# Kernel tuning notes

Hardware: AMD Instinct MI355X
Metric: run time of the kernel (lower is better)

The kernel has to match this reference:

```python
import jax, jax.numpy as jnp
import numpy as np

TOP_K = 4  # matches init kwarg top_k


def setup_inputs() -> dict:
    key = jax.random.key(0)
    k1, k2 = jax.random.split(key)
    G, S, D, E = 4, 2048, 1024, 32
    x = jax.random.normal(k1, (G, S, D), dtype=jnp.float32)
    W = jax.random.normal(k2, (D, E), dtype=jnp.float32) * (1.0 / np.sqrt(D))
    b = jnp.zeros((E,), dtype=jnp.float32)
    return {"x": x, "W": W, "b": b, "expert_capacity": 256}


def reference(x, W, b, expert_capacity):
    # gating_logits: [G, S, E]
    gating_logits = jnp.einsum('gsd,de->gse', x, W) + b
    gating_probs = jax.nn.softmax(gating_logits, axis=-1)
    # top-k gate values and expert indices: [G, S, K]
    expert_gate, expert_index = jax.lax.top_k(gating_probs, TOP_K)
    E = gating_probs.shape[2]
    # one-hot expert mask: [G, S, K, E]
    expert_mask = jax.nn.one_hot(expert_index, num_classes=E, dtype=gating_probs.dtype)
    # position of each assignment within its expert (1-based where assigned)
    position_in_expert = jnp.cumsum(expert_mask, axis=1) * expert_mask  # [G,S,K,E]
    valid_assignment = position_in_expert < expert_capacity
    expert_gate_valid = expert_gate[..., None] * valid_assignment.astype(expert_gate.dtype)
    # one-hot over capacity slots: [G,S,K,E,C]
    combine_per_assignment = expert_gate_valid[..., None] * jax.nn.one_hot(
        position_in_expert, num_classes=expert_capacity, dtype=expert_gate.dtype)
    combine_tensor = jnp.sum(combine_per_assignment, axis=2)  # [G,S,E,C]
    combine_tensor = combine_tensor[..., 1:]                  # drop slot 0 (unassigned)
    dispatch_mask = combine_tensor.astype(bool)
    loss = 0.0  # training=False
    return combine_tensor, dispatch_mask, loss
```

## Files before the change

kernel.cpp:

```cpp
#include <hip/hip_runtime.h>

#define G 4
#define S 2048
#define D 1024
#define E 32
#define TOPK 4
#define NTOK (G * S)
#define NROW (NTOK * E)
#define ROWLEN 255
#define HALF (NROW * ROWLEN)


__global__ __launch_bounds__(256) void gemm_topk_kernel(
    const float* __restrict__ x, const float* __restrict__ W,
    const float* __restrict__ b,
    float* __restrict__ gate_ws, int* __restrict__ idx_ws,
    int2* __restrict__ tab)
{
    const int tid   = threadIdx.x;
    const int token = blockIdx.x * 8 + (tid >> 5);
    const int e     = tid & 31;

    tab[token * E + e] = make_int2(0, 0);

    const float4* x4 = (const float4*)x;
    const long xb = (long)token * (D / 4);

    float acc = 0.f;
#pragma unroll 4
    for (int d4 = 0; d4 < D / 4; ++d4) {
        float4 xv = x4[xb + d4];
        const float* wp = W + d4 * 4 * E + e;
        acc = fmaf(xv.x, wp[0],     acc);
        acc = fmaf(xv.y, wp[E],     acc);
        acc = fmaf(xv.z, wp[2 * E], acc);
        acc = fmaf(xv.w, wp[3 * E], acc);
    }
    acc += b[e];

    float m = acc;
#pragma unroll
    for (int off = 16; off >= 1; off >>= 1)
        m = fmaxf(m, __shfl_xor(m, off, 32));
    float ex = __expf(acc - m);
    float sum = ex;
#pragma unroll
    for (int off = 16; off >= 1; off >>= 1)
        sum += __shfl_xor(sum, off, 32);
    float prob = ex / sum;

    const int g = token >> 11;
    const int s = token & (S - 1);

    float p = prob;
#pragma unroll
    for (int kk = 0; kk < TOPK; ++kk) {
        float v = p;
        int   vi = e;
#pragma unroll
        for (int off = 16; off >= 1; off >>= 1) {
            float ov = __shfl_xor(v, off, 32);
            int   oi = __shfl_xor(vi, off, 32);
            if (ov > v || (ov == v && oi < vi)) { v = ov; vi = oi; }
        }
        if (e == kk) {
            gate_ws[(kk * G + g) * S + s] = v;
            idx_ws [(kk * G + g) * S + s] = vi;
        }
        if (e == vi) p = -1.f;
    }
}

__global__ __launch_bounds__(64) void positions_kernel(
    const int* __restrict__ idx_ws, const float* __restrict__ gate_ws,
    const int* __restrict__ cap_ptr, int2* __restrict__ tab)
{
    const int row  = blockIdx.x;
    const int lane = threadIdx.x;
    const int cap  = *cap_ptr;
    const int g    = row & (G - 1);
    const int* idx = idx_ws + row * S;
    const float* gw = gate_ws + row * S;

    int cnt = 0;
    const unsigned long long lowmask = (1ull << lane) - 1ull;

    for (int c = 0; c < S / 64; ++c) {
        const int s  = c * 64 + lane;
        const int my = idx[s];
        unsigned long long eqm = 0ull, mycol = 0ull;
#pragma unroll
        for (int ee = 0; ee < E; ++ee) {
            unsigned long long bal = __ballot(my == ee);
            if (my == ee)   eqm   = bal;
            if (lane == ee) mycol = bal;
        }
        const int prior = __shfl(cnt, my);
        const int pos = prior + __popcll(eqm & lowmask) + 1;
        if (pos < cap) {
            tab[(g * S + s) * E + my] = make_int2(__float_as_int(gw[s]), pos);
        }
        cnt += __popcll(mycol);
    }
}

__global__ __launch_bounds__(256) void write_out_kernel(
    const int2* __restrict__ tab, float* __restrict__ out, int n)
{
    const int n4 = n >> 2;
    float4* out4 = (float4*)out;
    int i = blockIdx.x * blockDim.x + threadIdx.x;
    const int stride = gridDim.x * blockDim.x;

    for (; i < n4; i += stride) {
        const unsigned f = (unsigned)i << 2;
        const int region = f >= (unsigned)HALF;
        const unsigned fp = region ? f - (unsigned)HALF : f;
        const unsigned r  = fp / 255u;
        const int p0 = (int)(fp - r * 255u);

        const int2 e0 = tab[r];
        const int2 e1 = tab[r + 1];

        const float g0 = region ? 1.0f : __int_as_float(e0.x);
        const float g1 = region ? 1.0f : __int_as_float(e1.x);

        const int j0 = e0.y - 1 - p0;
        const int j1 = (e1.y > 0 && e1.y < 256) ? (e1.y + 254 - p0) : -1;

        float4 v;
        v.x = (j0 == 0) ? g0 : ((j1 == 0) ? g1 : 0.f);
        v.y = (j0 == 1) ? g0 : ((j1 == 1) ? g1 : 0.f);
        v.z = (j0 == 2) ? g0 : ((j1 == 2) ? g1 : 0.f);
        v.w = (j0 == 3) ? g0 : ((j1 == 3) ? g1 : 0.f);
        out4[i] = v;
    }
    if (blockIdx.x == 0 && threadIdx.x == 0) {
        for (int t = n4 << 2; t < n; ++t) out[t] = 0.f;
    }
}

extern "C" void kernel_launch(void* const* d_in, const int* in_sizes, int n_in,
                              void* d_out, int out_size, void* d_ws, size_t ws_size,
                              hipStream_t stream)
{
    const float* x   = (const float*)d_in[0];
    const float* W   = (const float*)d_in[1];
    const float* b   = (const float*)d_in[2];
    const int*   cap = (const int*)d_in[3];
    float* out = (float*)d_out;

    const int NA = G * S * TOPK;
    int2*  tab     = (int2*)d_ws;
    float* gate_ws = (float*)(tab + NROW + 8);
    int*   idx_ws  = (int*)(gate_ws + NA);

    gemm_topk_kernel<<<NTOK / 8, 256, 0, stream>>>(x, W, b, gate_ws, idx_ws, tab);
    positions_kernel<<<G * TOPK, 64, 0, stream>>>(idx_ws, gate_ws, cap, tab);
    write_out_kernel<<<8192, 256, 0, stream>>>(tab, out, out_size);
}
```

Measured before the change: 654.8 us.

## Zero output concurrently with gating GEMM and scatter nonzeros directly

```diff
diff --git a/kernel.cpp b/kernel.cpp
--- a/kernel.cpp
+++ b/kernel.cpp
@@ -9,19 +9,32 @@
 #define NROW (NTOK * E)
 #define ROWLEN 255
 #define HALF (NROW * ROWLEN)
+#define NFLOAT (2 * HALF + 1)
+#define GEMM_BLOCKS (NTOK / 8)
+#define ZERO_BLOCKS 8192
 
-
-__global__ __launch_bounds__(256) void gemm_topk_kernel(
+__global__ __launch_bounds__(256) void prep_kernel(
     const float* __restrict__ x, const float* __restrict__ W,
     const float* __restrict__ b,
     float* __restrict__ gate_ws, int* __restrict__ idx_ws,
-    int2* __restrict__ tab)
+    float* __restrict__ out)
 {
-    const int tid   = threadIdx.x;
+    const int tid = threadIdx.x;
+
+    if (blockIdx.x >= GEMM_BLOCKS) {
+        const int n4 = NFLOAT >> 2;
+        float4* out4 = (float4*)out;
+        int i = (blockIdx.x - GEMM_BLOCKS) * 256 + tid;
+        const int stride = ZERO_BLOCKS * 256;
+        const float4 z = make_float4(0.f, 0.f, 0.f, 0.f);
+        for (; i < n4; i += stride) out4[i] = z;
+        if (blockIdx.x == GEMM_BLOCKS && tid == 0)
+            out[NFLOAT - 1] = 0.f;
+        return;
+    }
+
     const int token = blockIdx.x * 8 + (tid >> 5);
     const int e     = tid & 31;
-
-    tab[token * E + e] = make_int2(0, 0);
 
     const float4* x4 = (const float4*)x;
     const long xb = (long)token * (D / 4);
@@ -71,9 +84,9 @@
     }
 }
 
-__global__ __launch_bounds__(64) void positions_kernel(
+__global__ __launch_bounds__(64) void positions_scatter_kernel(
     const int* __restrict__ idx_ws, const float* __restrict__ gate_ws,
-    const int* __restrict__ cap_ptr, int2* __restrict__ tab)
+    const int* __restrict__ cap_ptr, float* __restrict__ out)
 {
     const int row  = blockIdx.x;
     const int lane = threadIdx.x;
@@ -98,45 +111,11 @@
         const int prior = __shfl(cnt, my);
         const int pos = prior + __popcll(eqm & lowmask) + 1;
         if (pos < cap) {
-            tab[(g * S + s) * E + my] = make_int2(__float_as_int(gw[s]), pos);
+            const int off = ((g * S + s) * E + my) * ROWLEN + (pos - 1);
+            out[off]        = gw[s];
+            out[HALF + off] = 1.0f;
         }
         cnt += __popcll(mycol);
-    }
-}
-
-__global__ __launch_bounds__(256) void write_out_kernel(
-    const int2* __restrict__ tab, float* __restrict__ out, int n)
-{
-    const int n4 = n >> 2;
-    float4* out4 = (float4*)out;
-    int i = blockIdx.x * blockDim.x + threadIdx.x;
-    const int stride = gridDim.x * blockDim.x;
-
-    for (; i < n4; i += stride) {
-        const unsigned f = (unsigned)i << 2;
-        const int region = f >= (unsigned)HALF;
-        const unsigned fp = region ? f - (unsigned)HALF : f;
-        const unsigned r  = fp / 255u;
-        const int p0 = (int)(fp - r * 255u);
-
-        const int2 e0 = tab[r];
-        const int2 e1 = tab[r + 1];
-
-        const float g0 = region ? 1.0f : __int_as_float(e0.x);
-        const float g1 = region ? 1.0f : __int_as_float(e1.x);
-
-        const int j0 = e0.y - 1 - p0;
-        const int j1 = (e1.y > 0 && e1.y < 256) ? (e1.y + 254 - p0) : -1;
-
-        float4 v;
-        v.x = (j0 == 0) ? g0 : ((j1 == 0) ? g1 : 0.f);
-        v.y = (j0 == 1) ? g0 : ((j1 == 1) ? g1 : 0.f);
-        v.z = (j0 == 2) ? g0 : ((j1 == 2) ? g1 : 0.f);
-        v.w = (j0 == 3) ? g0 : ((j1 == 3) ? g1 : 0.f);
-        out4[i] = v;
-    }
-    if (blockIdx.x == 0 && threadIdx.x == 0) {
-        for (int t = n4 << 2; t < n; ++t) out[t] = 0.f;
     }
 }
 
@@ -151,11 +130,11 @@
     float* out = (float*)d_out;
 
     const int NA = G * S * TOPK;
-    int2*  tab     = (int2*)d_ws;
-    float* gate_ws = (float*)(tab + NROW + 8);
+    float* gate_ws = (float*)d_ws;
     int*   idx_ws  = (int*)(gate_ws + NA);
 
-    gemm_topk_kernel<<<NTOK / 8, 256, 0, stream>>>(x, W, b, gate_ws, idx_ws, tab);
-    positions_kernel<<<G * TOPK, 64, 0, stream>>>(idx_ws, gate_ws, cap, tab);
-    write_out_kernel<<<8192, 256, 0, stream>>>(tab, out, out_size);
+    prep_kernel<<<GEMM_BLOCKS + ZERO_BLOCKS, 256, 0, stream>>>(
+        x, W, b, gate_ws, idx_ws, out);
+    positions_scatter_kernel<<<G * TOPK, 64, 0, stream>>>(
+        idx_ws, gate_ws, cap, out);
 }
```

Result: slower. 670.8 us (+2.4%).
